# Kernel tuning notes

Hardware: AMD Instinct MI355X
Metric: run time of the kernel (lower is better)

The kernel has to match this reference:

```python
import jax, jax.numpy as jnp
import numpy as np

D_MODEL = 1024
NUM_HEADS = 16
HEAD_DIM = D_MODEL // NUM_HEADS


def setup_inputs() -> dict:
    key = jax.random.key(0)
    ks = jax.random.split(key, 9)
    s = 1.0 / np.sqrt(D_MODEL)
    return {
        "x": jax.random.normal(ks[0], (4, 2048, D_MODEL), dtype=jnp.float32),
        "Wq": jax.random.uniform(ks[1], (D_MODEL, D_MODEL), minval=-s, maxval=s, dtype=jnp.float32),
        "bq": jax.random.uniform(ks[2], (D_MODEL,), minval=-s, maxval=s, dtype=jnp.float32),
        "Wk": jax.random.uniform(ks[3], (D_MODEL, D_MODEL), minval=-s, maxval=s, dtype=jnp.float32),
        "bk": jax.random.uniform(ks[4], (D_MODEL,), minval=-s, maxval=s, dtype=jnp.float32),
        "Wv": jax.random.uniform(ks[5], (D_MODEL, D_MODEL), minval=-s, maxval=s, dtype=jnp.float32),
        "bv": jax.random.uniform(ks[6], (D_MODEL,), minval=-s, maxval=s, dtype=jnp.float32),
        "Wo": jax.random.uniform(ks[7], (D_MODEL, D_MODEL), minval=-s, maxval=s, dtype=jnp.float32),
        "bo": jax.random.uniform(ks[8], (D_MODEL,), minval=-s, maxval=s, dtype=jnp.float32),
    }


def reference(x, Wq, bq, Wk, bk, Wv, bv, Wo, bo):
    B, T, C = x.shape
    H, Dh = NUM_HEADS, HEAD_DIM
    # projections (nn.Linear applies x @ W^T + b)
    q = (x @ Wq.T + bq).reshape(B, T, H, Dh).transpose(0, 2, 1, 3)  # [B,H,T,Dh]
    k = (x @ Wk.T + bk).reshape(B, T, H, Dh).transpose(0, 2, 1, 3)
    v = (x @ Wv.T + bv).reshape(B, T, H, Dh).transpose(0, 2, 1, 3)
    scale = 1.0 / np.sqrt(Dh).astype(np.float32)
    att = jnp.einsum("bhqd,bhkd->bhqk", q, k) * scale  # [B,H,T,T]
    causal = jnp.tril(jnp.ones((T, T), dtype=bool))
    att = jnp.where(causal[None, None], att, -jnp.inf)
    att = jax.nn.softmax(att, axis=-1)
    # dropout is identity in eval mode
    out = jnp.einsum("bhqk,bhkd->bhqd", att, v)  # [B,H,T,Dh]
    out = out.transpose(0, 2, 1, 3).reshape(B, T, C)
    return out @ Wo.T + bo
```

## Files before the change

### kernel.cpp

```cpp
#include <hip/hip_runtime.h>
#include <stdint.h>

typedef __attribute__((ext_vector_type(8))) short short8;
typedef __attribute__((ext_vector_type(4))) short short4v;
typedef __attribute__((ext_vector_type(4))) float floatx4;

#define QSCALE 0.1803368801111f

__device__ __forceinline__ unsigned short f2bf(float f) {
  unsigned int u = __float_as_uint(f);
  unsigned int r = (u + 0x7FFFu + ((u >> 16) & 1u)) >> 16;
  return (unsigned short)r;
}

__device__ __forceinline__ unsigned int cvt_pk_bf16(float lo, float hi) {
  unsigned int r;
  asm("v_cvt_pk_bf16_f32 %0, %1, %2" : "=v"(r) : "v"(lo), "v"(hi));
  return r;
}

__device__ __forceinline__ void async_copy16(void* lds, const void* g) {
  __builtin_amdgcn_global_load_lds(
      (const __attribute__((address_space(1))) unsigned int*)g,
      (__attribute__((address_space(3))) unsigned int*)lds, 16, 0, 0);
}

__global__ __launch_bounds__(256) void f2ball_kernel(
    const float* __restrict__ x, unsigned short* __restrict__ xb,
    const float* __restrict__ w0, const float* __restrict__ w1,
    const float* __restrict__ w2, const float* __restrict__ w3,
    unsigned short* __restrict__ o0, unsigned short* __restrict__ o1,
    unsigned short* __restrict__ o2, unsigned short* __restrict__ o3) {
  const float* in;
  unsigned short* out;
  long i;
  if (blockIdx.x < 8192) {
    in = x;
    out = xb;
    i = (long)blockIdx.x * 256 + threadIdx.x;
  } else {
    int wb = blockIdx.x - 8192;
    int which = wb >> 10;
    in = (which == 0) ? w0 : (which == 1) ? w1 : (which == 2) ? w2 : w3;
    out = (which == 0) ? o0 : (which == 1) ? o1 : (which == 2) ? o2 : o3;
    i = (long)(wb & 1023) * 256 + threadIdx.x;
  }
  float4 v = ((const float4*)in)[i];
  short4v o;
  o[0] = (short)f2bf(v.x);
  o[1] = (short)f2bf(v.y);
  o[2] = (short)f2bf(v.z);
  o[3] = (short)f2bf(v.w);
  *(short4v*)(out + i * 4) = o;
}

__device__ __forceinline__ void gemm128_mainloop_db(
    const unsigned short* __restrict__ A, const unsigned short* __restrict__ Bt,
    int K, long brow, long bcol, unsigned short* As, unsigned short* Bs,
    floatx4 acc[4][4]) {
  const int tid = threadIdx.x;
  const int wave = tid >> 6;
  const int lane = tid & 63;
  const int wr = wave >> 1, wc = wave & 1;
  const int lr = lane & 15, lg = lane >> 4;

  const unsigned short* ga = A + (brow + (tid >> 2)) * (long)K + (tid & 3) * 8;
  const unsigned short* gb = Bt + (bcol + (tid >> 2)) * (long)K + (tid & 3) * 8;
  const int woff = wave * 512;
  const int a_off = (wr * 64 + lr) * 32 + lg * 8;
  const int b_off = (wc * 64 + lr) * 32 + lg * 8;

  async_copy16(As + woff, ga);
  async_copy16(As + woff + 2048, ga + (long)64 * K);
  async_copy16(Bs + woff, gb);
  async_copy16(Bs + woff + 2048, gb + (long)64 * K);
  ga += 32;
  gb += 32;
  __syncthreads();

  int buf = 0;
  for (int kt = 0; kt < K; kt += 32) {
    if (kt + 32 < K) {
      unsigned short* lA = As + (buf ^ 1) * 4096 + woff;
      unsigned short* lB = Bs + (buf ^ 1) * 4096 + woff;
      async_copy16(lA, ga);
      async_copy16(lA + 2048, ga + (long)64 * K);
      async_copy16(lB, gb);
      async_copy16(lB + 2048, gb + (long)64 * K);
      ga += 32;
      gb += 32;
    }
    const unsigned short* Ab = As + buf * 4096;
    const unsigned short* Bb = Bs + buf * 4096;
    short8 af[4], bf[4];
#pragma unroll
    for (int i = 0; i < 4; ++i) {
      af[i] = *(const short8*)(Ab + a_off + i * 512);
      bf[i] = *(const short8*)(Bb + b_off + i * 512);
    }
#pragma unroll
    for (int i = 0; i < 4; ++i)
#pragma unroll
      for (int j = 0; j < 4; ++j)
        acc[i][j] = __builtin_amdgcn_mfma_f32_16x16x32_bf16(af[i], bf[j], acc[i][j], 0, 0, 0);
    __syncthreads();
    buf ^= 1;
  }
}

__global__ __launch_bounds__(256, 4) void qkv_gemm(
    const unsigned short* __restrict__ xb, const unsigned short* __restrict__ wqkv,
    const float* __restrict__ bq, const float* __restrict__ bk,
    const float* __restrict__ bv, unsigned short* __restrict__ q_out,
    unsigned short* __restrict__ k_out, unsigned short* __restrict__ vt_out) {
  __shared__ unsigned short As[2 * 128 * 32];
  __shared__ unsigned short Bs[2 * 128 * 32];
  floatx4 zero = {0.f, 0.f, 0.f, 0.f};
  floatx4 acc[4][4];
#pragma unroll
  for (int i = 0; i < 4; ++i)
#pragma unroll
    for (int j = 0; j < 4; ++j) acc[i][j] = zero;

  long brow = (long)blockIdx.x * 128;
  long bcol = (long)blockIdx.y * 128;
  gemm128_mainloop_db(xb, wqkv, 1024, brow, bcol, As, Bs, acc);

  const int wave = threadIdx.x >> 6, lane = threadIdx.x & 63;
  const int wr = wave >> 1, wc = wave & 1, lr = lane & 15, lg = lane >> 4;
  const int kind = (int)(bcol >> 10);
  const float* bias = (kind == 0) ? bq : (kind == 1 ? bk : bv);
#pragma unroll
  for (int i = 0; i < 4; ++i)
#pragma unroll
    for (int j = 0; j < 4; ++j)
#pragma unroll
      for (int r = 0; r < 4; ++r) {
        int m = (int)brow + wr * 64 + i * 16 + lg * 4 + r;
        int n = (int)bcol + wc * 64 + j * 16 + lr;
        int f = n & 1023;
        float v = acc[i][j][r] + bias[f];
        if (kind == 0) v *= QSCALE;
        unsigned short o = f2bf(v);
        int h = f >> 6, d = f & 63;
        int b = m >> 11, t = m & 2047;
        long bh = (long)(b * 16 + h);
        if (kind == 0)
          q_out[(bh * 2048 + t) * 64 + d] = o;
        else if (kind == 1)
          k_out[(bh * 2048 + t) * 64 + d] = o;
        else
          vt_out[(bh * 64 + d) * 2048 + t] = o;
      }
}

__global__ __launch_bounds__(256, 4) void out_gemm(
    const unsigned short* __restrict__ ob, const unsigned short* __restrict__ wo,
    const float* __restrict__ bo, float* __restrict__ out) {
  __shared__ unsigned short As[2 * 128 * 32];
  __shared__ unsigned short Bs[2 * 128 * 32];
  floatx4 zero = {0.f, 0.f, 0.f, 0.f};
  floatx4 acc[4][4];
#pragma unroll
  for (int i = 0; i < 4; ++i)
#pragma unroll
    for (int j = 0; j < 4; ++j) acc[i][j] = zero;

  long brow = (long)blockIdx.x * 128;
  long bcol = (long)blockIdx.y * 128;
  gemm128_mainloop_db(ob, wo, 1024, brow, bcol, As, Bs, acc);

  const int wave = threadIdx.x >> 6, lane = threadIdx.x & 63;
  const int wr = wave >> 1, wc = wave & 1, lr = lane & 15, lg = lane >> 4;
#pragma unroll
  for (int i = 0; i < 4; ++i)
#pragma unroll
    for (int j = 0; j < 4; ++j)
#pragma unroll
      for (int r = 0; r < 4; ++r) {
        int m = (int)brow + wr * 64 + i * 16 + lg * 4 + r;
        int n = (int)bcol + wc * 64 + j * 16 + lr;
        out[(long)m * 1024 + n] = acc[i][j][r] + bo[n];
      }
}

__device__ __forceinline__ void stage_kv(char* __restrict__ Kb, char* __restrict__ Vb,
                                         const char* __restrict__ Kp,
                                         const char* __restrict__ Vt, int kv0,
                                         int tid) {
  const int wave = tid >> 6;
#pragma unroll
  for (int j = 0; j < 2; ++j) {
    int d = j * 256 + tid;
    int row = d >> 3, cc = d & 7;
    int gc = cc ^ (row & 7);
    const char* gk = Kp + (size_t)kv0 * 128 + row * 128 + gc * 16;
    async_copy16(Kb + (j * 256 + wave * 64) * 16, gk);
    const char* gv = Vt + (size_t)row * 4096 + (size_t)kv0 * 2 + gc * 16;
    async_copy16(Vb + (j * 256 + wave * 64) * 16, gv);
  }
}

__device__ __forceinline__ void attn_step(
    const char* __restrict__ Kb, const char* __restrict__ Vb,
    char* __restrict__ PTw, const short8 (&qf)[2][2],
    int kv0, int q0, int lr, int lg, bool diag,
    float (&m_i)[2], float (&l_i)[2], floatx4 (&accO)[2][4]) {
  floatx4 zero = {0.f, 0.f, 0.f, 0.f};
  const int x7 = lr & 7;
  floatx4 s[2][4];
  __builtin_amdgcn_s_setprio(1);
#pragma unroll
  for (int nt = 0; nt < 4; ++nt) {
    const char* kr = Kb + (nt * 16 + lr) * 128;
    short8 kf0 = *(const short8*)(kr + ((lg ^ x7) * 16));
    short8 kf1 = *(const short8*)(kr + (((4 + lg) ^ x7) * 16));
#pragma unroll
    for (int qa = 0; qa < 2; ++qa) {
      floatx4 a = zero;
      a = __builtin_amdgcn_mfma_f32_16x16x32_bf16(kf0, qf[qa][0], a, 0, 0, 0);
      a = __builtin_amdgcn_mfma_f32_16x16x32_bf16(kf1, qf[qa][1], a, 0, 0, 0);
      s[qa][nt] = a;
    }
  }
  __builtin_amdgcn_s_setprio(0);

  if (diag) {
#pragma unroll
    for (int qa = 0; qa < 2; ++qa) {
      const int q = q0 + qa * 16 + lr;
#pragma unroll
      for (int nt = 0; nt < 4; ++nt)
#pragma unroll
        for (int r = 0; r < 4; ++r) {
          int kvi = kv0 + nt * 16 + lg * 4 + r;
          if (kvi > q) s[qa][nt][r] = -1e30f;
        }
    }
  }

  float pmax[2];
#pragma unroll
  for (int qa = 0; qa < 2; ++qa) {
    float m0 = fmaxf(fmaxf(s[qa][0][0], s[qa][0][1]), fmaxf(s[qa][0][2], s[qa][0][3]));
    float m1 = fmaxf(fmaxf(s[qa][1][0], s[qa][1][1]), fmaxf(s[qa][1][2], s[qa][1][3]));
    float m2 = fmaxf(fmaxf(s[qa][2][0], s[qa][2][1]), fmaxf(s[qa][2][2], s[qa][2][3]));
    float m3 = fmaxf(fmaxf(s[qa][3][0], s[qa][3][1]), fmaxf(s[qa][3][2], s[qa][3][3]));
    pmax[qa] = fmaxf(fmaxf(m0, m1), fmaxf(m2, m3));
  }

  float g = fmaxf(pmax[0] - m_i[0], pmax[1] - m_i[1]);
  if (__any(g > 11.5f)) {
#pragma unroll
    for (int qa = 0; qa < 2; ++qa) {
      float mx = fmaxf(pmax[qa], __shfl_xor(pmax[qa], 16));
      mx = fmaxf(mx, __shfl_xor(mx, 32));
      float mnew = fmaxf(m_i[qa], mx);
      float scl = exp2f(m_i[qa] - mnew);
      m_i[qa] = mnew;
      l_i[qa] *= scl;
#pragma unroll
      for (int r = 0; r < 4; ++r) {
        float so = __shfl(scl, lg * 4 + r);
#pragma unroll
        for (int dt = 0; dt < 4; ++dt) accO[qa][dt][r] *= so;
      }
    }
  }

#pragma unroll
  for (int qa = 0; qa < 2; ++qa) {
    char* prow = PTw + (qa * 16 + lr) * 128;
#pragma unroll
    for (int nt = 0; nt < 4; ++nt) {
      float p0 = exp2f(s[qa][nt][0] - m_i[qa]);
      float p1 = exp2f(s[qa][nt][1] - m_i[qa]);
      float p2 = exp2f(s[qa][nt][2] - m_i[qa]);
      float p3 = exp2f(s[qa][nt][3] - m_i[qa]);
      l_i[qa] += (p0 + p1) + (p2 + p3);
      uint2 wv;
      wv.x = cvt_pk_bf16(p0, p1);
      wv.y = cvt_pk_bf16(p2, p3);
      *(uint2*)(prow + (((2 * nt + (lg >> 1)) ^ x7) * 16) + ((2 * lg) & 3) * 4) = wv;
    }
  }

  __builtin_amdgcn_s_setprio(1);
#pragma unroll
  for (int kk = 0; kk < 2; ++kk) {
    short8 pf0 = *(const short8*)(PTw + lr * 128 + (((4 * kk + lg) ^ x7) * 16));
    short8 pf1 = *(const short8*)(PTw + (16 + lr) * 128 + (((4 * kk + lg) ^ x7) * 16));
#pragma unroll
    for (int dt = 0; dt < 4; ++dt) {
      short8 vf = *(const short8*)(Vb + (dt * 16 + lr) * 128 + (((4 * kk + lg) ^ x7) * 16));
      accO[0][dt] = __builtin_amdgcn_mfma_f32_16x16x32_bf16(pf0, vf, accO[0][dt], 0, 0, 0);
      accO[1][dt] = __builtin_amdgcn_mfma_f32_16x16x32_bf16(pf1, vf, accO[1][dt], 0, 0, 0);
    }
  }
  __builtin_amdgcn_s_setprio(0);
}

__global__ __launch_bounds__(256, 2) void attn_fwd(
    const unsigned short* __restrict__ qb, const unsigned short* __restrict__ kb,
    const unsigned short* __restrict__ vtb, unsigned short* __restrict__ ob) {
  __shared__ __align__(16) char Kbuf[2][8192];
  __shared__ __align__(16) char Vbuf[2][8192];
  __shared__ __align__(16) char PTbuf[4][4096];

  const int bh = blockIdx.x * 8 + (blockIdx.y & 7);
  const int pr = blockIdx.y >> 3;

  const int tid = threadIdx.x;
  const int wave = tid >> 6, lane = tid & 63;
  const int lr = lane & 15, lg = lane >> 4;
  const unsigned short* Q = qb + (long)bh * 2048 * 64;
  const char* Kp = (const char*)(kb + (long)bh * 2048 * 64);
  const char* Vt = (const char*)(vtb + (long)bh * 64 * 2048);
  const int b = bh >> 4, h = bh & 15;
  char* PTw = PTbuf[wave];

  floatx4 zero = {0.f, 0.f, 0.f, 0.f};

#pragma unroll 1
  for (int half = 0; half < 2; ++half) {
    const int qt = half ? (15 - pr) : pr;
    const int q0 = qt * 128 + wave * 32;
    const int nkv = 2 * qt + 2;

    short8 qf[2][2];
#pragma unroll
    for (int qa = 0; qa < 2; ++qa)
#pragma unroll
      for (int kk = 0; kk < 2; ++kk)
        qf[qa][kk] = *(const short8*)(Q + (q0 + qa * 16 + lr) * 64 + kk * 32 + lg * 8);

    floatx4 accO[2][4];
#pragma unroll
    for (int qa = 0; qa < 2; ++qa)
#pragma unroll
      for (int dt = 0; dt < 4; ++dt) accO[qa][dt] = zero;
    float m_i[2] = {-1e30f, -1e30f};
    float l_i[2] = {0.f, 0.f};

    stage_kv(Kbuf[0], Vbuf[0], Kp, Vt, 0, tid);
    __syncthreads();
#pragma unroll 1
    for (int kv = 0; kv < nkv; ++kv) {
      if (kv + 1 < nkv)
        stage_kv(Kbuf[(kv + 1) & 1], Vbuf[(kv + 1) & 1], Kp, Vt, (kv + 1) * 64, tid);
      attn_step(Kbuf[kv & 1], Vbuf[kv & 1], PTw, qf, kv * 64, q0, lr, lg,
                kv >= 2 * qt, m_i, l_i, accO);
      __syncthreads();
    }

#pragma unroll
    for (int qa = 0; qa < 2; ++qa) {
      float lt = l_i[qa] + __shfl_xor(l_i[qa], 16);
      lt += __shfl_xor(lt, 32);
      float linv = 1.f / lt;
#pragma unroll
      for (int r = 0; r < 4; ++r) {
        float io = __shfl(linv, lg * 4 + r);
        int tq = q0 + qa * 16 + 4 * lg + r;
#pragma unroll
        for (int dt = 0; dt < 4; ++dt)
          ob[((long)b * 2048 + tq) * 1024 + h * 64 + dt * 16 + lr] =
              f2bf(accO[qa][dt][r] * io);
      }
    }
  }
}

extern "C" void kernel_launch(void* const* d_in, const int* in_sizes, int n_in,
                              void* d_out, int out_size, void* d_ws, size_t ws_size,
                              hipStream_t stream) {
  const float* x = (const float*)d_in[0];
  const float* bq = (const float*)d_in[2];
  const float* bk = (const float*)d_in[4];
  const float* bv = (const float*)d_in[6];
  const float* bo = (const float*)d_in[8];
  float* out = (float*)d_out;

  char* ws = (char*)d_ws;
  unsigned short* xb = (unsigned short*)(ws);
  unsigned short* wqkv = (unsigned short*)(ws + (16l << 20));
  unsigned short* wob = (unsigned short*)(ws + (22l << 20));
  unsigned short* qb = (unsigned short*)(ws + (24l << 20));
  unsigned short* kb = (unsigned short*)(ws + (40l << 20));
  unsigned short* vtb = (unsigned short*)(ws + (56l << 20));
  unsigned short* ob = (unsigned short*)(ws + (72l << 20));

  f2ball_kernel<<<12288, 256, 0, stream>>>(
      x, xb, (const float*)d_in[1], (const float*)d_in[3], (const float*)d_in[5],
      (const float*)d_in[7], wqkv, wqkv + (1l << 20), wqkv + (2l << 20), wob);

  qkv_gemm<<<dim3(64, 24), 256, 0, stream>>>(xb, wqkv, bq, bk, bv, qb, kb, vtb);
  attn_fwd<<<dim3(8, 64), 256, 0, stream>>>(qb, kb, vtb, ob);
  out_gemm<<<dim3(64, 8), 256, 0, stream>>>(ob, wob, bo, out);
}
```

Before: 192.0 us.

## Software-pipeline attention QK with softmax/PV and coalesce V-transpose stores via LDS

The attention loop moves to a triple-buffered K/V ring and splits each step into a QK tile and a softmax+PV part, so the QK MFMAs for the next tile are issued alongside the current tile's softmax and PV. Separately, the QKV GEMM epilogue for the V slice now stages the tile transposed in LDS and writes V^T with 16-byte coalesced stores instead of scattered 2-byte writes. This adds LDS use (an extra K/V buffer), more live registers for two score tiles, and extra syncs. The loop relies on nkv being even, since it always runs the second half-step.

```diff
diff --git a/kernel.cpp b/kernel.cpp
--- a/kernel.cpp
+++ b/kernel.cpp
@@ -113,8 +113,9 @@
     const float* __restrict__ bq, const float* __restrict__ bk,
     const float* __restrict__ bv, unsigned short* __restrict__ q_out,
     unsigned short* __restrict__ k_out, unsigned short* __restrict__ vt_out) {
-  __shared__ unsigned short As[2 * 128 * 32];
-  __shared__ unsigned short Bs[2 * 128 * 32];
+  __shared__ __align__(16) unsigned short Sh[128 * 136];
+  unsigned short* As = Sh;
+  unsigned short* Bs = Sh + 8192;
   floatx4 zero = {0.f, 0.f, 0.f, 0.f};
   floatx4 acc[4][4];
 #pragma unroll
@@ -130,28 +131,55 @@
   const int wr = wave >> 1, wc = wave & 1, lr = lane & 15, lg = lane >> 4;
   const int kind = (int)(bcol >> 10);
   const float* bias = (kind == 0) ? bq : (kind == 1 ? bk : bv);
-#pragma unroll
-  for (int i = 0; i < 4; ++i)
-#pragma unroll
-    for (int j = 0; j < 4; ++j)
-#pragma unroll
-      for (int r = 0; r < 4; ++r) {
-        int m = (int)brow + wr * 64 + i * 16 + lg * 4 + r;
-        int n = (int)bcol + wc * 64 + j * 16 + lr;
-        int f = n & 1023;
-        float v = acc[i][j][r] + bias[f];
-        if (kind == 0) v *= QSCALE;
-        unsigned short o = f2bf(v);
-        int h = f >> 6, d = f & 63;
-        int b = m >> 11, t = m & 2047;
-        long bh = (long)(b * 16 + h);
-        if (kind == 0)
-          q_out[(bh * 2048 + t) * 64 + d] = o;
-        else if (kind == 1)
-          k_out[(bh * 2048 + t) * 64 + d] = o;
-        else
-          vt_out[(bh * 64 + d) * 2048 + t] = o;
+
+  if (kind == 2) {
+#pragma unroll
+    for (int i = 0; i < 4; ++i)
+#pragma unroll
+      for (int j = 0; j < 4; ++j) {
+        int n_local = wc * 64 + j * 16 + lr;
+        int m_base = wr * 64 + i * 16 + lg * 4;
+        float bsc = bias[(int)((bcol + n_local) & 1023)];
+        short4v pk;
+#pragma unroll
+        for (int r = 0; r < 4; ++r) pk[r] = (short)f2bf(acc[i][j][r] + bsc);
+        *(short4v*)(Sh + n_local * 136 + m_base) = pk;
       }
+    __syncthreads();
+    const int b = (int)(brow >> 11);
+    const int t0 = (int)(brow & 2047);
+    const int f0 = (int)(bcol - 2048);
+#pragma unroll
+    for (int p = 0; p < 8; ++p) {
+      int c = p * 256 + threadIdx.x;
+      int d_loc = c >> 4, tc = c & 15;
+      short8 v = *(const short8*)(Sh + d_loc * 136 + tc * 8);
+      int h = (f0 >> 6) + (d_loc >> 6);
+      int d = d_loc & 63;
+      *(short8*)(vt_out + ((long)((b * 16 + h) * 64 + d)) * 2048 + t0 + tc * 8) = v;
+    }
+  } else {
+#pragma unroll
+    for (int i = 0; i < 4; ++i)
+#pragma unroll
+      for (int j = 0; j < 4; ++j)
+#pragma unroll
+        for (int r = 0; r < 4; ++r) {
+          int m = (int)brow + wr * 64 + i * 16 + lg * 4 + r;
+          int n = (int)bcol + wc * 64 + j * 16 + lr;
+          int f = n & 1023;
+          float v = acc[i][j][r] + bias[f];
+          if (kind == 0) v *= QSCALE;
+          unsigned short o = f2bf(v);
+          int h = f >> 6, d = f & 63;
+          int bb = m >> 11, t = m & 2047;
+          long bh = (long)(bb * 16 + h);
+          if (kind == 0)
+            q_out[(bh * 2048 + t) * 64 + d] = o;
+          else
+            k_out[(bh * 2048 + t) * 64 + d] = o;
+        }
+  }
 }
 
 __global__ __launch_bounds__(256, 4) void out_gemm(
@@ -201,14 +229,10 @@
   }
 }
 
-__device__ __forceinline__ void attn_step(
-    const char* __restrict__ Kb, const char* __restrict__ Vb,
-    char* __restrict__ PTw, const short8 (&qf)[2][2],
-    int kv0, int q0, int lr, int lg, bool diag,
-    float (&m_i)[2], float (&l_i)[2], floatx4 (&accO)[2][4]) {
+__device__ __forceinline__ void qk_tile(floatx4 (&s)[2][4], const char* __restrict__ Kb,
+                                        const short8 (&qf)[2][2], int lr, int lg) {
   floatx4 zero = {0.f, 0.f, 0.f, 0.f};
   const int x7 = lr & 7;
-  floatx4 s[2][4];
   __builtin_amdgcn_s_setprio(1);
 #pragma unroll
   for (int nt = 0; nt < 4; ++nt) {
@@ -224,7 +248,13 @@
     }
   }
   __builtin_amdgcn_s_setprio(0);
-
+}
+
+__device__ __forceinline__ void sm_pv(
+    floatx4 (&s)[2][4], const char* __restrict__ Vb, char* __restrict__ PTw,
+    int kv0, int q0, int lr, int lg, bool diag,
+    float (&m_i)[2], float (&l_i)[2], floatx4 (&accO)[2][4]) {
+  const int x7 = lr & 7;
   if (diag) {
 #pragma unroll
     for (int qa = 0; qa < 2; ++qa) {
@@ -303,8 +333,8 @@
 __global__ __launch_bounds__(256, 2) void attn_fwd(
     const unsigned short* __restrict__ qb, const unsigned short* __restrict__ kb,
     const unsigned short* __restrict__ vtb, unsigned short* __restrict__ ob) {
-  __shared__ __align__(16) char Kbuf[2][8192];
-  __shared__ __align__(16) char Vbuf[2][8192];
+  __shared__ __align__(16) char Kbuf[3][8192];
+  __shared__ __align__(16) char Vbuf[3][8192];
   __shared__ __align__(16) char PTbuf[4][4096];
 
   const int bh = blockIdx.x * 8 + (blockIdx.y & 7);
@@ -344,13 +374,23 @@
 
     stage_kv(Kbuf[0], Vbuf[0], Kp, Vt, 0, tid);
     __syncthreads();
+    stage_kv(Kbuf[1], Vbuf[1], Kp, Vt, 64, tid);
+    floatx4 sA[2][4], sB[2][4];
+    qk_tile(sA, Kbuf[0], qf, lr, lg);
+
 #pragma unroll 1
-    for (int kv = 0; kv < nkv; ++kv) {
-      if (kv + 1 < nkv)
-        stage_kv(Kbuf[(kv + 1) & 1], Vbuf[(kv + 1) & 1], Kp, Vt, (kv + 1) * 64, tid);
-      attn_step(Kbuf[kv & 1], Vbuf[kv & 1], PTw, qf, kv * 64, q0, lr, lg,
-                kv >= 2 * qt, m_i, l_i, accO);
+    for (int kv = 0; kv < nkv; kv += 2) {
       __syncthreads();
+      if (kv + 2 < nkv)
+        stage_kv(Kbuf[(kv + 2) % 3], Vbuf[(kv + 2) % 3], Kp, Vt, (kv + 2) * 64, tid);
+      qk_tile(sB, Kbuf[(kv + 1) % 3], qf, lr, lg);
+      sm_pv(sA, Vbuf[kv % 3], PTw, kv * 64, q0, lr, lg, kv >= 2 * qt, m_i, l_i, accO);
+      __syncthreads();
+      if (kv + 3 < nkv)
+        stage_kv(Kbuf[(kv + 3) % 3], Vbuf[(kv + 3) % 3], Kp, Vt, (kv + 3) * 64, tid);
+      if (kv + 2 < nkv) qk_tile(sA, Kbuf[(kv + 2) % 3], qf, lr, lg);
+      sm_pv(sB, Vbuf[(kv + 1) % 3], PTw, (kv + 1) * 64, q0, lr, lg, kv + 1 >= 2 * qt,
+            m_i, l_i, accO);
     }
 
 #pragma unroll
```

After: 171.9 us. 10.5% less time.
